# Kernel tuning notes

Measured on AMD Instinct MI355X. Metric: run time of the kernel, lower is better.

Reference implementation:

```python
import jax, jax.numpy as jnp
import numpy as np

B, T, D = 32, 1024, 192
HIDDEN = 4
CH = D * HIDDEN          # conv hidden channels = in_channel * hidden_size
K1, K2 = 5, 3
PAD = 3                  # (K1 - 1) // 2 + 1 for odd kernel_size=5 (ReplicationPad1d)
NUM_LEVELS = 3
N_NODES = 2 ** NUM_LEVELS - 1  # 7 Interaction blocks in the SCINet tree
OUT_LEN = 512


def setup_inputs() -> dict:
    key = jax.random.key(0)
    ks = jax.random.split(key, 6)
    s1 = 1.0 / np.sqrt(D * K1)   # torch Conv1d default init bound (fan_in = Cin*k)
    s2 = 1.0 / np.sqrt(CH * K2)
    sp = 1.0 / np.sqrt(T)
    x = jax.random.normal(ks[0], (B, T, D), dtype=jnp.float32)
    # Stacked params for all 7 tree nodes x 4 branches (phi, psi, eta, rho)
    W1 = jax.random.uniform(ks[1], (N_NODES, 4, CH, D, K1), jnp.float32, -s1, s1)
    b1 = jax.random.uniform(ks[2], (N_NODES, 4, CH), jnp.float32, -s1, s1)
    W2 = jax.random.uniform(ks[3], (N_NODES, 4, D, CH, K2), jnp.float32, -s2, s2)
    b2 = jax.random.uniform(ks[4], (N_NODES, 4, D), jnp.float32, -s2, s2)
    # projection1 = Conv1d(input_len, output_len, k=1, bias=False) over time-as-channels
    Wproj = jax.random.uniform(ks[5], (OUT_LEN, T), jnp.float32, -sp, sp)
    return {"x": x, "W1": W1, "b1": b1, "W2": W2, "b2": b2, "Wproj": Wproj}


def _conv1d(x, w, b):
    # x: (B, Cin, L), w: (Cout, Cin, K)
    y = jax.lax.conv_general_dilated(x, w, (1,), 'VALID',
                                     dimension_numbers=('NCH', 'OIH', 'NCH'))
    return y + b[None, :, None]


def _branch(x, w1, b1, w2, b2):
    # ReplicationPad1d(3,3) -> Conv(k=5) -> LeakyReLU -> (Dropout p=0) -> Conv(k=3) -> Tanh
    xp = jnp.pad(x, ((0, 0), (0, 0), (PAD, PAD)), mode='edge')
    h = jax.nn.leaky_relu(_conv1d(xp, w1, b1), 0.01)
    return jnp.tanh(_conv1d(h, w2, b2))  # length back to L


def _interact(x, w1, b1, w2, b2):
    # x: (B, T, D) -> even/odd (B, D, T/2)
    xe = jnp.transpose(x[:, ::2, :], (0, 2, 1))
    xo = jnp.transpose(x[:, 1::2, :], (0, 2, 1))
    d = xo * jnp.exp(_branch(xe, w1[0], b1[0], w2[0], b2[0]))  # phi
    c = xe * jnp.exp(_branch(xo, w1[1], b1[1], w2[1], b2[1]))  # psi
    even_up = c + _branch(d, w1[2], b1[2], w2[2], b2[2])        # eta
    odd_up = d - _branch(c, w1[3], b1[3], w2[3], b2[3])         # rho
    return jnp.transpose(even_up, (0, 2, 1)), jnp.transpose(odd_up, (0, 2, 1))


def _zip_up(even, odd):
    # interleave even/odd along time (equal lengths since T % 2**levels == 0)
    b, t, c = even.shape
    return jnp.stack([even, odd], axis=2).reshape(b, 2 * t, c)


def _tree(x, level, idx, W1, b1, W2, b2):
    i = idx[0]
    idx[0] += 1
    e, o = _interact(x, W1[i], b1[i], W2[i], b2[i])
    if level == 0:
        return _zip_up(e, o)
    return _zip_up(_tree(e, level - 1, idx, W1, b1, W2, b2),
                   _tree(o, level - 1, idx, W1, b1, W2, b2))


def reference(x, W1, b1, W2, b2, Wproj):
    out = _tree(x, NUM_LEVELS - 1, [0], W1, b1, W2, b2) + x  # residual
    # projection1: Conv1d over time-as-channels, kernel 1, no bias
    return jnp.einsum('btd,ot->bod', out, Wproj)
```

## Files before the change

### kernel.cpp

```cpp
#include <hip/hip_runtime.h>
#include <hip/hip_bf16.h>

typedef unsigned short u16;
typedef unsigned int u32;
typedef __bf16 bf16x8 __attribute__((ext_vector_type(8)));
typedef float f32x4 __attribute__((ext_vector_type(4)));

#define NB 32
#define NT 1024
#define ND 192
#define NCH 768
#define NOUT 512

__device__ __forceinline__ float bf2f(u16 x) { return __uint_as_float(((u32)x) << 16); }
__device__ __forceinline__ u16 f2bf(float f) {
    u32 u = __float_as_uint(f);
    return (u16)((u + 0x7fffu + ((u >> 16) & 1u)) >> 16);
}
__device__ __forceinline__ float tanh_fast(float x) {
    float e = __expf(2.f * x);
    return 1.f - 2.f / (e + 1.f);
}
__device__ __forceinline__ int xcd_swz(int bx, int nwg) {
    int q = nwg >> 3, r = nwg & 7;
    int xcd = bx & 7, idx = bx >> 3;
    return (xcd < r ? xcd * (q + 1) : r * (q + 1) + (xcd - r) * q) + idx;
}

__constant__ int NODE_IDX[3][4] = {{0, 0, 0, 0}, {1, 4, 0, 0}, {2, 5, 3, 6}};

__global__ void cvt8(const float* __restrict__ in, u16* __restrict__ out, int n8) {
    int i = blockIdx.x * 256 + threadIdx.x;
    if (i >= n8) return;
    const float4* p = (const float4*)in + 2 * (size_t)i;
    float4 a = p[0], c = p[1];
    uint4 o;
    o.x = f2bf(a.x) | ((u32)f2bf(a.y) << 16);
    o.y = f2bf(a.z) | ((u32)f2bf(a.w) << 16);
    o.z = f2bf(c.x) | ((u32)f2bf(c.y) << 16);
    o.w = f2bf(c.z) | ((u32)f2bf(c.w) << 16);
    ((uint4*)out)[i] = o;
}

__global__ __launch_bounds__(256) void w1fk(const float* __restrict__ W1, u16* __restrict__ W1f) {
    __shared__ u16 ls[32][968];
    const int nb = blockIdx.x / 24;
    const int cot = blockIdx.x % 24;
    const float* src = W1 + ((size_t)nb * NCH + cot * 32) * (ND * 5);
    for (int idx = threadIdx.x; idx < 7680; idx += 256) {
        int e4 = idx * 4;
        int rowc = e4 / 960, col = e4 % 960;
        float4 v = *(const float4*)(src + (size_t)rowc * 960 + col);
        ls[rowc][col + 0] = f2bf(v.x);
        ls[rowc][col + 1] = f2bf(v.y);
        ls[rowc][col + 2] = f2bf(v.z);
        ls[rowc][col + 3] = f2bf(v.w);
    }
    __syncthreads();
    const int lane = threadIdx.x & 63, sub = threadIdx.x >> 6;
    const int g = lane >> 4, r = lane & 15;
    for (int it = 0; it < 15; ++it) {
        int fid = it * 4 + sub;
        int kkb = fid >> 1, cobl = fid & 1;
        u16 tmp[8];
#pragma unroll
        for (int e = 0; e < 8; ++e) {
            int kk = kkb * 32 + 8 * g + e;
            int ci = kk % 192, k = kk / 192;
            tmp[e] = ls[cobl * 16 + r][ci * 5 + k];
        }
        uint4 o;
        o.x = tmp[0] | ((u32)tmp[1] << 16);
        o.y = tmp[2] | ((u32)tmp[3] << 16);
        o.z = tmp[4] | ((u32)tmp[5] << 16);
        o.w = tmp[6] | ((u32)tmp[7] << 16);
        size_t off = (((size_t)nb * 30 + kkb) * 48 + cot * 2 + cobl) * 512 + lane * 8;
        *(uint4*)(W1f + off) = o;
    }
}

__global__ __launch_bounds__(256) void w2fk(const float* __restrict__ W2, u16* __restrict__ W2f) {
    __shared__ u16 ls[16][1160];
    const int ch = blockIdx.x & 1;
    const int t = blockIdx.x >> 1;
    const int nb = t / 12, cot = t % 12;
    const float* src = W2 + ((size_t)nb * ND + cot * 16) * (NCH * 3) + ch * 1152;
    for (int idx = threadIdx.x; idx < 4608; idx += 256) {
        int e4 = idx * 4;
        int rowc = e4 / 1152, col = e4 % 1152;
        float4 v = *(const float4*)(src + (size_t)rowc * (NCH * 3) + col);
        ls[rowc][col + 0] = f2bf(v.x);
        ls[rowc][col + 1] = f2bf(v.y);
        ls[rowc][col + 2] = f2bf(v.z);
        ls[rowc][col + 3] = f2bf(v.w);
    }
    __syncthreads();
    const int lane = threadIdx.x & 63, sub = threadIdx.x >> 6;
    const int g = lane >> 4, r = lane & 15;
    for (int it = 0; it < 9; ++it) {
        int fid = it * 4 + sub;
        int k = fid / 12, cib = fid % 12;
        int kkb = k * 24 + ch * 12 + cib;
        u16 tmp[8];
#pragma unroll
        for (int e = 0; e < 8; ++e) {
            int cl = cib * 32 + 8 * g + e;
            tmp[e] = ls[r][cl * 3 + k];
        }
        uint4 o;
        o.x = tmp[0] | ((u32)tmp[1] << 16);
        o.y = tmp[2] | ((u32)tmp[3] << 16);
        o.z = tmp[4] | ((u32)tmp[5] << 16);
        o.w = tmp[6] | ((u32)tmp[7] << 16);
        size_t off = (((size_t)nb * 72 + kkb) * 12 + cot) * 512 + lane * 8;
        *(uint4*)(W2f + off) = o;
    }
}

__global__ __launch_bounds__(256) void conv1m(
    const u16* __restrict__ bufb, const u16* __restrict__ dbufb, const u16* __restrict__ cbufb,
    const u16* __restrict__ W1f, const float* __restrict__ b1,
    u16* __restrict__ h, int lvl, int stage) {
    const int L = 512 >> lvl, nodes = 1 << lvl, Lout = L + 2;
    const int tid = threadIdx.x;
    const int mT1 = (NB * Lout + 63) / 64;
    const int wg = xcd_swz(blockIdx.x, gridDim.x);
    const int z = wg / (6 * mT1);
    const int rem = wg - z * 6 * mT1;
    const int mt = rem / 6;
    const int cot = rem % 6;
    const int g_node = z & (nodes - 1);
    const int br = z >> lvl;
    const int nb4 = NODE_IDX[lvl][g_node] * 4 + (stage ? 2 + br : br);

    const int r0 = mt * 64;
    const int b0 = r0 / Lout;
    const int t00 = r0 - b0 * Lout;
    const int s = Lout - t00;
    const int rowsValid0 = NB * Lout - r0;
    const int rowsValid = rowsValid0 < 64 ? rowsValid0 : 64;

    __shared__ u16 xs[72 * 192];

    const u16* dcb = br ? cbufb : dbufb;
    const int slot = g_node + (br << lvl);
    for (int ch = tid; ch < 72 * 24; ch += 256) {
        int j = ch / 24, c8 = ch % 24;
        int bb, u;
        if (j <= s + 3) { bb = b0; u = t00 - 3 + j; }
        else            { bb = b0 + 1; u = j - s - 7; }
        u = u < 0 ? 0 : (u > L - 1 ? L - 1 : u);
        if (bb > NB - 1) bb = NB - 1;
        const u16* p;
        if (stage == 0)
            p = bufb + ((size_t)bb * NT + slot + (size_t)u * (2 * nodes)) * ND + c8 * 8;
        else
            p = dcb + (((size_t)g_node * NB + bb) * L + u) * (size_t)ND + c8 * 8;
        *(uint4*)(xs + j * 192 + ((c8 * 8) ^ ((j & 7) << 3))) = *(const uint4*)p;
    }
    __syncthreads();

    const int lane = tid & 63, w = tid >> 6;
    const int lr = lane & 15, lg = lane >> 4;

    int rowb[4];
#pragma unroll
    for (int m = 0; m < 4; ++m) {
        int i = m * 16 + lr;
        rowb[m] = i + (i >= s ? 4 : 0);
    }
    const u16* wf = W1f + (size_t)nb4 * 30 * 48 * 512 + (size_t)(cot * 8 + w * 2) * 512 + lane * 8;

    f32x4 acc[4][2];
    f32x4 zz = {0.f, 0.f, 0.f, 0.f};
#pragma unroll
    for (int m = 0; m < 4; ++m)
#pragma unroll
        for (int n = 0; n < 2; ++n) acc[m][n] = zz;

    auto loadA = [&](bf16x8(&dst)[4], int step) {
        const int k = step / 6, cib = step % 6;
#pragma unroll
        for (int m = 0; m < 4; ++m) {
            int row = rowb[m] + k;
            int idx = row * 192 + ((cib * 32 + lg * 8) ^ ((row & 7) << 3));
            dst[m] = *(const bf16x8*)(xs + idx);
        }
    };
    auto loadB = [&](bf16x8(&dst)[2], int step) {
#pragma unroll
        for (int n = 0; n < 2; ++n)
            dst[n] = *(const bf16x8*)(wf + ((size_t)step * 48 + n) * 512);
    };
    auto domfma = [&](bf16x8(&A)[4], bf16x8(&B)[2]) {
#pragma unroll
        for (int m = 0; m < 4; ++m)
#pragma unroll
            for (int n = 0; n < 2; ++n)
                acc[m][n] = __builtin_amdgcn_mfma_f32_16x16x32_bf16(A[m], B[n], acc[m][n], 0, 0, 0);
    };

    bf16x8 Ab[2][4], Bb[3][2];
    loadA(Ab[0], 0);
    loadB(Bb[0], 0);
    loadB(Bb[1], 1);
#pragma unroll
    for (int sp = 0; sp < 30; ++sp) {
        if (sp + 2 < 30) loadB(Bb[(sp + 2) % 3], sp + 2);
        if (sp + 1 < 30) loadA(Ab[(sp + 1) & 1], sp + 1);
        domfma(Ab[sp & 1], Bb[sp % 3]);
    }

    float bias[2];
    const float* bb1 = b1 + (size_t)nb4 * NCH + cot * 128 + w * 32 + lr;
#pragma unroll
    for (int n = 0; n < 2; ++n) bias[n] = bb1[n * 16];
    u16* hz = h + (size_t)z * NB * Lout * NCH;
#pragma unroll
    for (int m = 0; m < 4; ++m) {
#pragma unroll
        for (int rr = 0; rr < 4; ++rr) {
            int i = m * 16 + lg * 4 + rr;
            if (i < rowsValid) {
                int cross = (i >= s) ? 1 : 0;
                int bb = b0 + cross;
                int tt = cross ? i - s : t00 + i;
                u16* dst = hz + ((size_t)bb * Lout + tt) * NCH + cot * 128 + w * 32 + lr;
#pragma unroll
                for (int n = 0; n < 2; ++n) {
                    float v = acc[m][n][rr] + bias[n];
                    v = v > 0.f ? v : 0.01f * v;
                    dst[n * 16] = f2bf(v);
                }
            }
        }
    }
}

__global__ __launch_bounds__(256) void conv2m(
    u16* __restrict__ bufb, u16* __restrict__ dbufb, u16* __restrict__ cbufb,
    const u16* __restrict__ W2f, const float* __restrict__ b2,
    const u16* __restrict__ h, int lvl, int stage) {
    const int L = 512 >> lvl, nodes = 1 << lvl, Lout = L + 2;
    const int tid = threadIdx.x;
    const int nM = (NB * L) >> 6;
    const int wg = xcd_swz(blockIdx.x, gridDim.x);
    const int z = wg / (nM * 2);
    const int rem = wg - z * nM * 2;
    const int mt = rem >> 1;
    const int nh = rem & 1;
    const int g_node = z & (nodes - 1);
    const int br = z >> lvl;
    const int nb4 = NODE_IDX[lvl][g_node] * 4 + (stage ? 2 + br : br);
    const int r0 = mt * 64;
    const int b = r0 >> (9 - lvl);
    const int t0 = r0 & (L - 1);

    __shared__ u16 xs[66 * 192];
    const u16* hz = h + ((size_t)z * NB + b) * Lout * NCH;

    const int lane = tid & 63, w = tid >> 6;
    const int wrow = w >> 1, wcol = w & 1;
    const int lr = lane & 15, lg = lane >> 4;
    int rowb[2];
#pragma unroll
    for (int m = 0; m < 2; ++m) rowb[m] = wrow * 32 + m * 16 + lr;
    const u16* wf = W2f + (size_t)nb4 * 72 * 12 * 512 + (size_t)(nh * 6 + wcol * 3) * 512 + lane * 8;

    f32x4 acc[2][3];
    f32x4 zz = {0.f, 0.f, 0.f, 0.f};
#pragma unroll
    for (int m = 0; m < 2; ++m)
#pragma unroll
        for (int n = 0; n < 3; ++n) acc[m][n] = zz;

    for (int cc = 0; cc < 4; ++cc) {
        __syncthreads();
        for (int ch = tid; ch < 66 * 24; ch += 256) {
            int j = ch / 24, c8 = ch % 24;
            *(uint4*)(xs + j * 192 + ((c8 * 8) ^ ((j & 7) << 3))) =
                *(const uint4*)(hz + (size_t)(t0 + j) * NCH + cc * 192 + c8 * 8);
        }
        __syncthreads();

        auto loadA = [&](bf16x8(&dst)[2], int step) {
            const int k = step / 6, cib = step % 6;
#pragma unroll
            for (int m = 0; m < 2; ++m) {
                int row = rowb[m] + k;
                int idx = row * 192 + ((cib * 32 + lg * 8) ^ ((row & 7) << 3));
                dst[m] = *(const bf16x8*)(xs + idx);
            }
        };
        auto loadB = [&](bf16x8(&dst)[3], int step) {
            const int k = step / 6, cib = step % 6;
            const size_t kb = (size_t)(cc * 6 + k * 24 + cib) * 12 * 512;
#pragma unroll
            for (int n = 0; n < 3; ++n)
                dst[n] = *(const bf16x8*)(wf + kb + (size_t)n * 512);
        };
        auto domfma = [&](bf16x8(&A)[2], bf16x8(&B)[3]) {
#pragma unroll
            for (int m = 0; m < 2; ++m)
#pragma unroll
                for (int n = 0; n < 3; ++n)
                    acc[m][n] = __builtin_amdgcn_mfma_f32_16x16x32_bf16(A[m], B[n], acc[m][n], 0, 0, 0);
        };

        bf16x8 Ab[2][2], Bb[3][3];
        loadA(Ab[0], 0);
        loadB(Bb[0], 0);
        loadB(Bb[1], 1);
#pragma unroll
        for (int sp = 0; sp < 18; ++sp) {
            if (sp + 2 < 18) loadB(Bb[(sp + 2) % 3], sp + 2);
            if (sp + 1 < 18) loadA(Ab[(sp + 1) & 1], sp + 1);
            domfma(Ab[sp & 1], Bb[sp % 3]);
        }
    }

    float bias[3];
    const float* bb2 = b2 + (size_t)nb4 * ND + nh * 96 + wcol * 48 + lr;
#pragma unroll
    for (int n = 0; n < 3; ++n) bias[n] = bb2[n * 16];

    const int tstr = 2 * nodes;
    if (stage == 0) {
        const int mo = g_node + (br == 0 ? nodes : 0);
        const u16* mult = bufb + ((size_t)b * NT + mo) * ND;
        u16* dst = (br == 0 ? dbufb : cbufb) + ((size_t)g_node * NB + b) * (size_t)L * ND;
#pragma unroll
        for (int m = 0; m < 2; ++m) {
#pragma unroll
            for (int rr = 0; rr < 4; ++rr) {
                int i = wrow * 32 + m * 16 + lg * 4 + rr;
                int t = t0 + i;
#pragma unroll
                for (int n = 0; n < 3; ++n) {
                    int co = nh * 96 + wcol * 48 + n * 16 + lr;
                    float v = tanh_fast(acc[m][n][rr] + bias[n]);
                    float mlt = bf2f(mult[(size_t)t * tstr * ND + co]);
                    dst[(size_t)t * ND + co] = f2bf(mlt * __expf(v));
                }
            }
        }
    } else {
        const u16* other = (br == 0 ? cbufb : dbufb) + ((size_t)g_node * NB + b) * (size_t)L * ND;
        const int to = g_node + (br ? nodes : 0);
        u16* dst = bufb + ((size_t)b * NT + to) * ND;
#pragma unroll
        for (int m = 0; m < 2; ++m) {
#pragma unroll
            for (int rr = 0; rr < 4; ++rr) {
                int i = wrow * 32 + m * 16 + lg * 4 + rr;
                int t = t0 + i;
#pragma unroll
                for (int n = 0; n < 3; ++n) {
                    int co = nh * 96 + wcol * 48 + n * 16 + lr;
                    float v = tanh_fast(acc[m][n][rr] + bias[n]);
                    float o = bf2f(other[(size_t)t * ND + co]);
                    dst[(size_t)t * tstr * ND + co] = f2bf(br == 0 ? o + v : o - v);
                }
            }
        }
    }
}

__global__ __launch_bounds__(256) void mkin2T(const u16* __restrict__ bufb,
                                              const float* __restrict__ x,
                                              u16* __restrict__ in2T) {
    __shared__ u16 ls[64][72];
    const int b = blockIdx.z, t0 = blockIdx.y * 64, d0 = blockIdx.x * 64;
    const int tid = threadIdx.x;
#pragma unroll
    for (int it = 0; it < 2; ++it) {
        int idx = tid + it * 256;
        int c8 = idx >> 6, row = idx & 63;
        size_t base = ((size_t)b * NT + t0 + row) * ND + d0 + c8 * 8;
        uint4 vb = *(const uint4*)(bufb + base);
        float4 x1 = *(const float4*)(x + base);
        float4 x2 = *(const float4*)(x + base + 4);
        const u16* vs = (const u16*)&vb;
        ls[c8 * 8 + 0][row] = f2bf(bf2f(vs[0]) + x1.x);
        ls[c8 * 8 + 1][row] = f2bf(bf2f(vs[1]) + x1.y);
        ls[c8 * 8 + 2][row] = f2bf(bf2f(vs[2]) + x1.z);
        ls[c8 * 8 + 3][row] = f2bf(bf2f(vs[3]) + x1.w);
        ls[c8 * 8 + 4][row] = f2bf(bf2f(vs[4]) + x2.x);
        ls[c8 * 8 + 5][row] = f2bf(bf2f(vs[5]) + x2.y);
        ls[c8 * 8 + 6][row] = f2bf(bf2f(vs[6]) + x2.z);
        ls[c8 * 8 + 7][row] = f2bf(bf2f(vs[7]) + x2.w);
    }
    __syncthreads();
#pragma unroll
    for (int it = 0; it < 2; ++it) {
        int idx = tid + it * 256;
        int dl = idx >> 3, t8 = idx & 7;
        uint4 v = *(uint4*)&ls[dl][t8 * 8];
        *(uint4*)(in2T + ((size_t)b * ND + d0 + dl) * NT + t0 + t8 * 8) = v;
    }
}

__global__ __launch_bounds__(256) void projm(const u16* __restrict__ in2T,
                                             const u16* __restrict__ Wpb,
                                             float* __restrict__ out) {
    const int b = blockIdx.y, ot = blockIdx.x;
    const int tid = threadIdx.x, lane = tid & 63, w = tid >> 6;
    const int lr = lane & 15, lg = lane >> 4;
    const u16* ap = Wpb + ((size_t)(ot * 32 + lr)) * NT + lg * 8;
    const u16* bp = in2T + ((size_t)b * ND + w * 48 + lr) * NT + lg * 8;

    f32x4 acc[2][3];
    f32x4 zz = {0.f, 0.f, 0.f, 0.f};
#pragma unroll
    for (int m = 0; m < 2; ++m)
#pragma unroll
        for (int n = 0; n < 3; ++n) acc[m][n] = zz;

    auto loadA = [&](bf16x8(&dst)[2], int kkb) {
#pragma unroll
        for (int m = 0; m < 2; ++m)
            dst[m] = *(const bf16x8*)(ap + (size_t)m * 16 * NT + kkb * 32);
    };
    auto loadB = [&](bf16x8(&dst)[3], int kkb) {
#pragma unroll
        for (int n = 0; n < 3; ++n)
            dst[n] = *(const bf16x8*)(bp + (size_t)n * 16 * NT + kkb * 32);
    };
    auto domfma = [&](bf16x8(&A)[2], bf16x8(&B)[3]) {
#pragma unroll
        for (int m = 0; m < 2; ++m)
#pragma unroll
            for (int n = 0; n < 3; ++n)
                acc[m][n] = __builtin_amdgcn_mfma_f32_16x16x32_bf16(A[m], B[n], acc[m][n], 0, 0, 0);
    };

    bf16x8 Ab[2][2], Bb[3][3];
    loadA(Ab[0], 0);
    loadB(Bb[0], 0);
    loadB(Bb[1], 1);
#pragma unroll
    for (int sp = 0; sp < 32; ++sp) {
        if (sp + 2 < 32) loadB(Bb[(sp + 2) % 3], sp + 2);
        if (sp + 1 < 32) loadA(Ab[(sp + 1) & 1], sp + 1);
        domfma(Ab[sp & 1], Bb[sp % 3]);
    }

#pragma unroll
    for (int m = 0; m < 2; ++m)
#pragma unroll
        for (int rr = 0; rr < 4; ++rr) {
            int o = ot * 32 + m * 16 + lg * 4 + rr;
#pragma unroll
            for (int n = 0; n < 3; ++n) {
                int d = w * 48 + n * 16 + lr;
                out[((size_t)b * NOUT + o) * ND + d] = acc[m][n][rr];
            }
        }
}

extern "C" void kernel_launch(void* const* d_in, const int* in_sizes, int n_in,
                              void* d_out, int out_size, void* d_ws, size_t ws_size,
                              hipStream_t stream) {
    const float* x = (const float*)d_in[0];
    const float* W1 = (const float*)d_in[1];
    const float* b1 = (const float*)d_in[2];
    const float* W2 = (const float*)d_in[3];
    const float* b2 = (const float*)d_in[4];
    const float* Wp = (const float*)d_in[5];
    float* out = (float*)d_out;

    char* wsb = (char*)d_ws;
    size_t off = 0;
    auto carve = [&](size_t bytes) {
        void* p = wsb + off;
        off += (bytes + 255) & ~(size_t)255;
        return p;
    };
    const size_t w1f_e = (size_t)28 * 30 * 48 * 512;
    const size_t w2f_e = (size_t)28 * 72 * 12 * 512;
    const size_t wpb_e = (size_t)NOUT * NT;
    const size_t buf_e = (size_t)NB * NT * ND;
    const size_t dc_e = (size_t)NB * 512 * ND;
    const size_t h_e = (size_t)1040 * NB * NCH;
    const size_t i2_e = (size_t)NB * ND * NT;

    u16* W1f = (u16*)carve(sizeof(u16) * w1f_e);
    u16* W2f = (u16*)carve(sizeof(u16) * w2f_e);
    u16* Wpb = (u16*)carve(sizeof(u16) * wpb_e);
    u16* bufb = (u16*)carve(sizeof(u16) * buf_e);
    u16* dbufb = (u16*)carve(sizeof(u16) * dc_e);
    u16* cbufb = (u16*)carve(sizeof(u16) * dc_e);
    u16* h = (u16*)carve(sizeof(u16) * h_e);
    u16* in2T = (u16*)carve(sizeof(u16) * i2_e);
    if (off > ws_size) return;

    cvt8<<<(int)(buf_e / 8 / 256), 256, 0, stream>>>(x, bufb, (int)(buf_e / 8));
    cvt8<<<(int)(wpb_e / 8 / 256), 256, 0, stream>>>(Wp, Wpb, (int)(wpb_e / 8));
    w1fk<<<28 * 24, 256, 0, stream>>>(W1, W1f);
    w2fk<<<28 * 12 * 2, 256, 0, stream>>>(W2, W2f);

    for (int lvl = 0; lvl < 3; ++lvl) {
        int L = 512 >> lvl, nodes = 1 << lvl, Lout = L + 2;
        int mT1 = (NB * Lout + 63) / 64;
        int nM = NB * L / 64;
        dim3 g1(6 * mT1 * 2 * nodes);
        dim3 g2(nM * 2 * 2 * nodes);
        conv1m<<<g1, 256, 0, stream>>>(bufb, dbufb, cbufb, W1f, b1, h, lvl, 0);
        conv2m<<<g2, 256, 0, stream>>>(bufb, dbufb, cbufb, W2f, b2, h, lvl, 0);
        conv1m<<<g1, 256, 0, stream>>>(bufb, dbufb, cbufb, W1f, b1, h, lvl, 1);
        conv2m<<<g2, 256, 0, stream>>>(bufb, dbufb, cbufb, W2f, b2, h, lvl, 1);
    }
    mkin2T<<<dim3(3, 16, NB), 256, 0, stream>>>(bufb, x, in2T);
    projm<<<dim3(16, NB), 256, 0, stream>>>(in2T, Wpb, out);
}
```

Measured before the change: 778.4 us.

## Enlarge conv GEMM tiles and stage weights into LDS via direct global-to-LDS loads

conv1m now computes 128-row by 128-channel tiles, with four waves in a 2x2 grid, where it used 64 rows. conv2m drops the output-channel split so each block covers all 192 output channels over 64 rows. In both kernels the weight fragments are double-buffered in LDS using global_load_lds, so one staged B tile is shared by all waves instead of each wave reading it from global memory. The aim is fewer weight reloads per FLOP and fewer A-tile rebuilds, at the cost of a __syncthreads on every k-step, more LDS, fewer blocks and added launch-bounds occupancy hints.

```diff
diff --git a/kernel.cpp b/kernel.cpp
--- a/kernel.cpp
+++ b/kernel.cpp
@@ -25,6 +25,11 @@
     int q = nwg >> 3, r = nwg & 7;
     int xcd = bx & 7, idx = bx >> 3;
     return (xcd < r ? xcd * (q + 1) : r * (q + 1) + (xcd - r) * q) + idx;
+}
+__device__ __forceinline__ void gl_lds16(const u16* g, u16* l) {
+    __builtin_amdgcn_global_load_lds(
+        (const __attribute__((address_space(1))) void*)g,
+        (__attribute__((address_space(3))) void*)l, 16, 0, 0);
 }
 
 __constant__ int NODE_IDX[3][4] = {{0, 0, 0, 0}, {1, 4, 0, 0}, {2, 5, 3, 6}};
@@ -117,13 +122,13 @@
     }
 }
 
-__global__ __launch_bounds__(256) void conv1m(
+__global__ __launch_bounds__(256, 2) void conv1m(
     const u16* __restrict__ bufb, const u16* __restrict__ dbufb, const u16* __restrict__ cbufb,
     const u16* __restrict__ W1f, const float* __restrict__ b1,
     u16* __restrict__ h, int lvl, int stage) {
     const int L = 512 >> lvl, nodes = 1 << lvl, Lout = L + 2;
     const int tid = threadIdx.x;
-    const int mT1 = (NB * Lout + 63) / 64;
+    const int mT1 = (NB * Lout + 127) / 128;
     const int wg = xcd_swz(blockIdx.x, gridDim.x);
     const int z = wg / (6 * mT1);
     const int rem = wg - z * 6 * mT1;
@@ -133,18 +138,19 @@
     const int br = z >> lvl;
     const int nb4 = NODE_IDX[lvl][g_node] * 4 + (stage ? 2 + br : br);
 
-    const int r0 = mt * 64;
+    const int r0 = mt * 128;
     const int b0 = r0 / Lout;
     const int t00 = r0 - b0 * Lout;
     const int s = Lout - t00;
     const int rowsValid0 = NB * Lout - r0;
-    const int rowsValid = rowsValid0 < 64 ? rowsValid0 : 64;
-
-    __shared__ u16 xs[72 * 192];
+    const int rowsValid = rowsValid0 < 128 ? rowsValid0 : 128;
+
+    __shared__ u16 xs[136 * 192];
+    __shared__ u16 bs[2][4096];
 
     const u16* dcb = br ? cbufb : dbufb;
     const int slot = g_node + (br << lvl);
-    for (int ch = tid; ch < 72 * 24; ch += 256) {
+    for (int ch = tid; ch < 136 * 24; ch += 256) {
         int j = ch / 24, c8 = ch % 24;
         int bb, u;
         if (j <= s + 3) { bb = b0; u = t00 - 3 + j; }
@@ -158,76 +164,73 @@
             p = dcb + (((size_t)g_node * NB + bb) * L + u) * (size_t)ND + c8 * 8;
         *(uint4*)(xs + j * 192 + ((c8 * 8) ^ ((j & 7) << 3))) = *(const uint4*)p;
     }
+
+    const u16* wsrc = W1f + ((size_t)nb4 * 30 * 48 + cot * 8) * 512;
+    auto stageB = [&](int kkb, int buf) {
+        const u16* gp = wsrc + (size_t)kkb * (48 * 512) + tid * 8;
+        u16* lp = &bs[buf][tid * 8];
+        gl_lds16(gp, lp);
+        gl_lds16(gp + 2048, lp + 2048);
+    };
+    stageB(0, 0);
     __syncthreads();
 
     const int lane = tid & 63, w = tid >> 6;
+    const int wrow = w >> 1, wcol = w & 1;
     const int lr = lane & 15, lg = lane >> 4;
 
     int rowb[4];
 #pragma unroll
     for (int m = 0; m < 4; ++m) {
-        int i = m * 16 + lr;
+        int i = wrow * 64 + m * 16 + lr;
         rowb[m] = i + (i >= s ? 4 : 0);
     }
-    const u16* wf = W1f + (size_t)nb4 * 30 * 48 * 512 + (size_t)(cot * 8 + w * 2) * 512 + lane * 8;
-
-    f32x4 acc[4][2];
+
+    f32x4 acc[4][4];
     f32x4 zz = {0.f, 0.f, 0.f, 0.f};
 #pragma unroll
     for (int m = 0; m < 4; ++m)
 #pragma unroll
-        for (int n = 0; n < 2; ++n) acc[m][n] = zz;
-
-    auto loadA = [&](bf16x8(&dst)[4], int step) {
-        const int k = step / 6, cib = step % 6;
+        for (int n = 0; n < 4; ++n) acc[m][n] = zz;
+
+#pragma unroll
+    for (int kkb = 0; kkb < 30; ++kkb) {
+        if (kkb < 29) stageB(kkb + 1, (kkb + 1) & 1);
+        const int k = kkb / 6, cib = kkb % 6;
+        bf16x8 Af[4], Bf[4];
 #pragma unroll
         for (int m = 0; m < 4; ++m) {
             int row = rowb[m] + k;
-            int idx = row * 192 + ((cib * 32 + lg * 8) ^ ((row & 7) << 3));
-            dst[m] = *(const bf16x8*)(xs + idx);
-        }
-    };
-    auto loadB = [&](bf16x8(&dst)[2], int step) {
-#pragma unroll
-        for (int n = 0; n < 2; ++n)
-            dst[n] = *(const bf16x8*)(wf + ((size_t)step * 48 + n) * 512);
-    };
-    auto domfma = [&](bf16x8(&A)[4], bf16x8(&B)[2]) {
+            Af[m] = *(const bf16x8*)(xs + row * 192 + ((cib * 32 + lg * 8) ^ ((row & 7) << 3)));
+        }
+#pragma unroll
+        for (int n = 0; n < 4; ++n)
+            Bf[n] = *(const bf16x8*)(&bs[kkb & 1][(wcol * 4 + n) * 512 + lane * 8]);
 #pragma unroll
         for (int m = 0; m < 4; ++m)
 #pragma unroll
-            for (int n = 0; n < 2; ++n)
-                acc[m][n] = __builtin_amdgcn_mfma_f32_16x16x32_bf16(A[m], B[n], acc[m][n], 0, 0, 0);
-    };
-
-    bf16x8 Ab[2][4], Bb[3][2];
-    loadA(Ab[0], 0);
-    loadB(Bb[0], 0);
-    loadB(Bb[1], 1);
-#pragma unroll
-    for (int sp = 0; sp < 30; ++sp) {
-        if (sp + 2 < 30) loadB(Bb[(sp + 2) % 3], sp + 2);
-        if (sp + 1 < 30) loadA(Ab[(sp + 1) & 1], sp + 1);
-        domfma(Ab[sp & 1], Bb[sp % 3]);
-    }
-
-    float bias[2];
-    const float* bb1 = b1 + (size_t)nb4 * NCH + cot * 128 + w * 32 + lr;
-#pragma unroll
-    for (int n = 0; n < 2; ++n) bias[n] = bb1[n * 16];
+            for (int n = 0; n < 4; ++n)
+                acc[m][n] = __builtin_amdgcn_mfma_f32_16x16x32_bf16(Af[m], Bf[n], acc[m][n], 0, 0, 0);
+        __syncthreads();
+    }
+
+    float bias[4];
+    const float* bb1 = b1 + (size_t)nb4 * NCH + cot * 128 + wcol * 64 + lr;
+#pragma unroll
+    for (int n = 0; n < 4; ++n) bias[n] = bb1[n * 16];
     u16* hz = h + (size_t)z * NB * Lout * NCH;
 #pragma unroll
     for (int m = 0; m < 4; ++m) {
 #pragma unroll
         for (int rr = 0; rr < 4; ++rr) {
-            int i = m * 16 + lg * 4 + rr;
+            int i = wrow * 64 + m * 16 + lg * 4 + rr;
             if (i < rowsValid) {
                 int cross = (i >= s) ? 1 : 0;
                 int bb = b0 + cross;
                 int tt = cross ? i - s : t00 + i;
-                u16* dst = hz + ((size_t)bb * Lout + tt) * NCH + cot * 128 + w * 32 + lr;
-#pragma unroll
-                for (int n = 0; n < 2; ++n) {
+                u16* dst = hz + ((size_t)bb * Lout + tt) * NCH + cot * 128 + wcol * 64 + lr;
+#pragma unroll
+                for (int n = 0; n < 4; ++n) {
                     float v = acc[m][n][rr] + bias[n];
                     v = v > 0.f ? v : 0.01f * v;
                     dst[n * 16] = f2bf(v);
@@ -237,7 +240,7 @@
     }
 }
 
-__global__ __launch_bounds__(256) void conv2m(
+__global__ __launch_bounds__(256, 3) void conv2m(
     u16* __restrict__ bufb, u16* __restrict__ dbufb, u16* __restrict__ cbufb,
     const u16* __restrict__ W2f, const float* __restrict__ b2,
     const u16* __restrict__ h, int lvl, int stage) {
@@ -245,10 +248,8 @@
     const int tid = threadIdx.x;
     const int nM = (NB * L) >> 6;
     const int wg = xcd_swz(blockIdx.x, gridDim.x);
-    const int z = wg / (nM * 2);
-    const int rem = wg - z * nM * 2;
-    const int mt = rem >> 1;
-    const int nh = rem & 1;
+    const int z = wg / nM;
+    const int mt = wg - z * nM;
     const int g_node = z & (nodes - 1);
     const int br = z >> lvl;
     const int nb4 = NODE_IDX[lvl][g_node] * 4 + (stage ? 2 + br : br);
@@ -257,70 +258,64 @@
     const int t0 = r0 & (L - 1);
 
     __shared__ u16 xs[66 * 192];
+    __shared__ u16 bs[2][6144];
     const u16* hz = h + ((size_t)z * NB + b) * Lout * NCH;
 
     const int lane = tid & 63, w = tid >> 6;
-    const int wrow = w >> 1, wcol = w & 1;
     const int lr = lane & 15, lg = lane >> 4;
-    int rowb[2];
-#pragma unroll
-    for (int m = 0; m < 2; ++m) rowb[m] = wrow * 32 + m * 16 + lr;
-    const u16* wf = W2f + (size_t)nb4 * 72 * 12 * 512 + (size_t)(nh * 6 + wcol * 3) * 512 + lane * 8;
-
-    f32x4 acc[2][3];
+
+    const u16* wsrc = W2f + (size_t)nb4 * 72 * 12 * 512;
+    auto stageB = [&](int kkb, int buf) {
+        const u16* gp = wsrc + (size_t)kkb * (12 * 512) + tid * 8;
+        u16* lp = &bs[buf][tid * 8];
+        gl_lds16(gp, lp);
+        gl_lds16(gp + 2048, lp + 2048);
+        gl_lds16(gp + 4096, lp + 4096);
+    };
+
+    f32x4 acc[4][3];
     f32x4 zz = {0.f, 0.f, 0.f, 0.f};
 #pragma unroll
-    for (int m = 0; m < 2; ++m)
+    for (int m = 0; m < 4; ++m)
 #pragma unroll
         for (int n = 0; n < 3; ++n) acc[m][n] = zz;
 
     for (int cc = 0; cc < 4; ++cc) {
         __syncthreads();
+        stageB(cc * 6, 0);
         for (int ch = tid; ch < 66 * 24; ch += 256) {
             int j = ch / 24, c8 = ch % 24;
             *(uint4*)(xs + j * 192 + ((c8 * 8) ^ ((j & 7) << 3))) =
                 *(const uint4*)(hz + (size_t)(t0 + j) * NCH + cc * 192 + c8 * 8);
         }
         __syncthreads();
-
-        auto loadA = [&](bf16x8(&dst)[2], int step) {
-            const int k = step / 6, cib = step % 6;
-#pragma unroll
-            for (int m = 0; m < 2; ++m) {
-                int row = rowb[m] + k;
-                int idx = row * 192 + ((cib * 32 + lg * 8) ^ ((row & 7) << 3));
-                dst[m] = *(const bf16x8*)(xs + idx);
+#pragma unroll
+        for (int sp = 0; sp < 18; ++sp) {
+            if (sp < 17) {
+                int spn = sp + 1;
+                stageB((spn / 6) * 24 + cc * 6 + (spn % 6), spn & 1);
             }
-        };
-        auto loadB = [&](bf16x8(&dst)[3], int step) {
-            const int k = step / 6, cib = step % 6;
-            const size_t kb = (size_t)(cc * 6 + k * 24 + cib) * 12 * 512;
+            const int k = sp / 6, cib = sp % 6;
+            bf16x8 Af[4], Bf[3];
+#pragma unroll
+            for (int m = 0; m < 4; ++m) {
+                int row = m * 16 + lr + k;
+                Af[m] = *(const bf16x8*)(xs + row * 192 + ((cib * 32 + lg * 8) ^ ((row & 7) << 3)));
+            }
 #pragma unroll
             for (int n = 0; n < 3; ++n)
-                dst[n] = *(const bf16x8*)(wf + kb + (size_t)n * 512);
-        };
-        auto domfma = [&](bf16x8(&A)[2], bf16x8(&B)[3]) {
-#pragma unroll
-            for (int m = 0; m < 2; ++m)
+                Bf[n] = *(const bf16x8*)(&bs[sp & 1][(w * 3 + n) * 512 + lane * 8]);
+#pragma unroll
+            for (int m = 0; m < 4; ++m)
 #pragma unroll
                 for (int n = 0; n < 3; ++n)
-                    acc[m][n] = __builtin_amdgcn_mfma_f32_16x16x32_bf16(A[m], B[n], acc[m][n], 0, 0, 0);
-        };
-
-        bf16x8 Ab[2][2], Bb[3][3];
-        loadA(Ab[0], 0);
-        loadB(Bb[0], 0);
-        loadB(Bb[1], 1);
-#pragma unroll
-        for (int sp = 0; sp < 18; ++sp) {
-            if (sp + 2 < 18) loadB(Bb[(sp + 2) % 3], sp + 2);
-            if (sp + 1 < 18) loadA(Ab[(sp + 1) & 1], sp + 1);
-            domfma(Ab[sp & 1], Bb[sp % 3]);
+                    acc[m][n] = __builtin_amdgcn_mfma_f32_16x16x32_bf16(Af[m], Bf[n], acc[m][n], 0, 0, 0);
+            __syncthreads();
         }
     }
 
     float bias[3];
-    const float* bb2 = b2 + (size_t)nb4 * ND + nh * 96 + wcol * 48 + lr;
+    const float* bb2 = b2 + (size_t)nb4 * ND + w * 48 + lr;
 #pragma unroll
     for (int n = 0; n < 3; ++n) bias[n] = bb2[n * 16];
 
@@ -330,14 +325,14 @@
         const u16* mult = bufb + ((size_t)b * NT + mo) * ND;
         u16* dst = (br == 0 ? dbufb : cbufb) + ((size_t)g_node * NB + b) * (size_t)L * ND;
 #pragma unroll
-        for (int m = 0; m < 2; ++m) {
+        for (int m = 0; m < 4; ++m) {
 #pragma unroll
             for (int rr = 0; rr < 4; ++rr) {
-                int i = wrow * 32 + m * 16 + lg * 4 + rr;
+                int i = m * 16 + lg * 4 + rr;
                 int t = t0 + i;
 #pragma unroll
                 for (int n = 0; n < 3; ++n) {
-                    int co = nh * 96 + wcol * 48 + n * 16 + lr;
+                    int co = w * 48 + n * 16 + lr;
                     float v = tanh_fast(acc[m][n][rr] + bias[n]);
                     float mlt = bf2f(mult[(size_t)t * tstr * ND + co]);
                     dst[(size_t)t * ND + co] = f2bf(mlt * __expf(v));
@@ -349,14 +344,14 @@
         const int to = g_node + (br ? nodes : 0);
         u16* dst = bufb + ((size_t)b * NT + to) * ND;
 #pragma unroll
-        for (int m = 0; m < 2; ++m) {
+        for (int m = 0; m < 4; ++m) {
 #pragma unroll
             for (int rr = 0; rr < 4; ++rr) {
-                int i = wrow * 32 + m * 16 + lg * 4 + rr;
+                int i = m * 16 + lg * 4 + rr;
                 int t = t0 + i;
 #pragma unroll
                 for (int n = 0; n < 3; ++n) {
-                    int co = nh * 96 + wcol * 48 + n * 16 + lr;
+                    int co = w * 48 + n * 16 + lr;
                     float v = tanh_fast(acc[m][n][rr] + bias[n]);
                     float o = bf2f(other[(size_t)t * ND + co]);
                     dst[(size_t)t * tstr * ND + co] = f2bf(br == 0 ? o + v : o - v);
@@ -501,10 +496,10 @@
 
     for (int lvl = 0; lvl < 3; ++lvl) {
         int L = 512 >> lvl, nodes = 1 << lvl, Lout = L + 2;
-        int mT1 = (NB * Lout + 63) / 64;
+        int mT1 = (NB * Lout + 127) / 128;
         int nM = NB * L / 64;
         dim3 g1(6 * mT1 * 2 * nodes);
-        dim3 g2(nM * 2 * 2 * nodes);
+        dim3 g2(nM * 2 * nodes);
         conv1m<<<g1, 256, 0, stream>>>(bufb, dbufb, cbufb, W1f, b1, h, lvl, 0);
         conv2m<<<g2, 256, 0, stream>>>(bufb, dbufb, cbufb, W2f, b2, h, lvl, 0);
         conv1m<<<g1, 256, 0, stream>>>(bufb, dbufb, cbufb, W1f, b1, h, lvl, 1);
```

After: 927.7 us. 19.2% more time.

## Switch conv GEMMs to 32x32x16 MFMA with larger tiles and repacked weights

Applied to the files above, without the earlier changes.

Both convolution GEMM kernels move from 16x16x32 to 32x32x16 bf16 MFMA instructions, and the weight-prepacking kernels are rewritten to emit fragments in the matching 32-row layout. conv1m doubles its M tile to 128 rows, which raises reuse of the shared input tile. conv2m drops the N-half split, so each block computes all 192 output channels and the hidden activations are loaded once instead of twice. The larger tiles give fewer workgroups and higher register and LDS use per block, which may reduce occupancy at the smaller tree levels.

```diff
diff --git a/kernel.cpp b/kernel.cpp
--- a/kernel.cpp
+++ b/kernel.cpp
@@ -5,6 +5,7 @@
 typedef unsigned int u32;
 typedef __bf16 bf16x8 __attribute__((ext_vector_type(8)));
 typedef float f32x4 __attribute__((ext_vector_type(4)));
+typedef float f32x16 __attribute__((ext_vector_type(16)));
 
 #define NB 32
 #define NT 1024
@@ -58,36 +59,35 @@
     }
     __syncthreads();
     const int lane = threadIdx.x & 63, sub = threadIdx.x >> 6;
-    const int g = lane >> 4, r = lane & 15;
+    const int r = lane & 31, g = lane >> 5;
     for (int it = 0; it < 15; ++it) {
-        int fid = it * 4 + sub;
-        int kkb = fid >> 1, cobl = fid & 1;
+        int kkb2 = it * 4 + sub;
         u16 tmp[8];
 #pragma unroll
         for (int e = 0; e < 8; ++e) {
-            int kk = kkb * 32 + 8 * g + e;
+            int kk = kkb2 * 16 + 8 * g + e;
             int ci = kk % 192, k = kk / 192;
-            tmp[e] = ls[cobl * 16 + r][ci * 5 + k];
+            tmp[e] = ls[r][ci * 5 + k];
         }
         uint4 o;
         o.x = tmp[0] | ((u32)tmp[1] << 16);
         o.y = tmp[2] | ((u32)tmp[3] << 16);
         o.z = tmp[4] | ((u32)tmp[5] << 16);
         o.w = tmp[6] | ((u32)tmp[7] << 16);
-        size_t off = (((size_t)nb * 30 + kkb) * 48 + cot * 2 + cobl) * 512 + lane * 8;
+        size_t off = (((size_t)nb * 60 + kkb2) * 24 + cot) * 512 + lane * 8;
         *(uint4*)(W1f + off) = o;
     }
 }
 
 __global__ __launch_bounds__(256) void w2fk(const float* __restrict__ W2, u16* __restrict__ W2f) {
-    __shared__ u16 ls[16][1160];
-    const int ch = blockIdx.x & 1;
-    const int t = blockIdx.x >> 1;
-    const int nb = t / 12, cot = t % 12;
-    const float* src = W2 + ((size_t)nb * ND + cot * 16) * (NCH * 3) + ch * 1152;
+    __shared__ u16 ls[32][579];
+    const int nb = blockIdx.x / 24;
+    const int rem = blockIdx.x % 24;
+    const int cob2 = rem / 4, ch = rem % 4;
+    const float* src = W2 + ((size_t)nb * ND + cob2 * 32) * (NCH * 3) + ch * 576;
     for (int idx = threadIdx.x; idx < 4608; idx += 256) {
         int e4 = idx * 4;
-        int rowc = e4 / 1152, col = e4 % 1152;
+        int rowc = e4 / 576, col = e4 % 576;
         float4 v = *(const float4*)(src + (size_t)rowc * (NCH * 3) + col);
         ls[rowc][col + 0] = f2bf(v.x);
         ls[rowc][col + 1] = f2bf(v.y);
@@ -96,23 +96,23 @@
     }
     __syncthreads();
     const int lane = threadIdx.x & 63, sub = threadIdx.x >> 6;
-    const int g = lane >> 4, r = lane & 15;
+    const int r = lane & 31, g = lane >> 5;
     for (int it = 0; it < 9; ++it) {
         int fid = it * 4 + sub;
-        int k = fid / 12, cib = fid % 12;
-        int kkb = k * 24 + ch * 12 + cib;
+        int k = fid / 12, cj = fid % 12;
+        int kkb2 = k * 48 + ch * 12 + cj;
         u16 tmp[8];
 #pragma unroll
         for (int e = 0; e < 8; ++e) {
-            int cl = cib * 32 + 8 * g + e;
-            tmp[e] = ls[r][cl * 3 + k];
+            int c_loc = cj * 16 + 8 * g + e;
+            tmp[e] = ls[r][c_loc * 3 + k];
         }
         uint4 o;
         o.x = tmp[0] | ((u32)tmp[1] << 16);
         o.y = tmp[2] | ((u32)tmp[3] << 16);
         o.z = tmp[4] | ((u32)tmp[5] << 16);
         o.w = tmp[6] | ((u32)tmp[7] << 16);
-        size_t off = (((size_t)nb * 72 + kkb) * 12 + cot) * 512 + lane * 8;
+        size_t off = (((size_t)nb * 144 + kkb2) * 6 + cob2) * 512 + lane * 8;
         *(uint4*)(W2f + off) = o;
     }
 }
@@ -123,7 +123,7 @@
     u16* __restrict__ h, int lvl, int stage) {
     const int L = 512 >> lvl, nodes = 1 << lvl, Lout = L + 2;
     const int tid = threadIdx.x;
-    const int mT1 = (NB * Lout + 63) / 64;
+    const int mT1 = (NB * Lout + 127) / 128;
     const int wg = xcd_swz(blockIdx.x, gridDim.x);
     const int z = wg / (6 * mT1);
     const int rem = wg - z * 6 * mT1;
@@ -133,18 +133,18 @@
     const int br = z >> lvl;
     const int nb4 = NODE_IDX[lvl][g_node] * 4 + (stage ? 2 + br : br);
 
-    const int r0 = mt * 64;
+    const int r0 = mt * 128;
     const int b0 = r0 / Lout;
     const int t00 = r0 - b0 * Lout;
     const int s = Lout - t00;
     const int rowsValid0 = NB * Lout - r0;
-    const int rowsValid = rowsValid0 < 64 ? rowsValid0 : 64;
-
-    __shared__ u16 xs[72 * 192];
+    const int rowsValid = rowsValid0 < 128 ? rowsValid0 : 128;
+
+    __shared__ u16 xs[136 * 192];
 
     const u16* dcb = br ? cbufb : dbufb;
     const int slot = g_node + (br << lvl);
-    for (int ch = tid; ch < 72 * 24; ch += 256) {
+    for (int ch = tid; ch < 136 * 24; ch += 256) {
         int j = ch / 24, c8 = ch % 24;
         int bb, u;
         if (j <= s + 3) { bb = b0; u = t00 - 3 + j; }
@@ -158,79 +158,80 @@
             p = dcb + (((size_t)g_node * NB + bb) * L + u) * (size_t)ND + c8 * 8;
         *(uint4*)(xs + j * 192 + ((c8 * 8) ^ ((j & 7) << 3))) = *(const uint4*)p;
     }
+
+    const int lane = tid & 63, w = tid >> 6;
+    const int wrow = w >> 1, wcol = w & 1;
+    const int l31 = lane & 31, lg2 = lane >> 5;
+
+    int rowb[2];
+#pragma unroll
+    for (int m = 0; m < 2; ++m) {
+        int i = wrow * 64 + m * 32 + l31;
+        rowb[m] = i + (i >= s ? 4 : 0);
+    }
+    const u16* wf = W1f + ((size_t)nb4 * 60 * 24 + cot * 4 + wcol * 2) * 512 + lane * 8;
+
     __syncthreads();
 
-    const int lane = tid & 63, w = tid >> 6;
-    const int lr = lane & 15, lg = lane >> 4;
-
-    int rowb[4];
-#pragma unroll
-    for (int m = 0; m < 4; ++m) {
-        int i = m * 16 + lr;
-        rowb[m] = i + (i >= s ? 4 : 0);
-    }
-    const u16* wf = W1f + (size_t)nb4 * 30 * 48 * 512 + (size_t)(cot * 8 + w * 2) * 512 + lane * 8;
-
-    f32x4 acc[4][2];
-    f32x4 zz = {0.f, 0.f, 0.f, 0.f};
-#pragma unroll
-    for (int m = 0; m < 4; ++m)
-#pragma unroll
-        for (int n = 0; n < 2; ++n) acc[m][n] = zz;
-
-    auto loadA = [&](bf16x8(&dst)[4], int step) {
-        const int k = step / 6, cib = step % 6;
-#pragma unroll
-        for (int m = 0; m < 4; ++m) {
-            int row = rowb[m] + k;
-            int idx = row * 192 + ((cib * 32 + lg * 8) ^ ((row & 7) << 3));
-            dst[m] = *(const bf16x8*)(xs + idx);
-        }
-    };
-    auto loadB = [&](bf16x8(&dst)[2], int step) {
+    f32x16 acc[2][2];
+#pragma unroll
+    for (int m = 0; m < 2; ++m)
+#pragma unroll
+        for (int n = 0; n < 2; ++n) acc[m][n] = (f32x16)0.f;
+
+    auto loadA = [&](bf16x8(&dst)[2], int st) {
+        const int kc = st / 12, cij = st % 12;
+        const int ci0 = cij * 16 + lg2 * 8;
+#pragma unroll
+        for (int m = 0; m < 2; ++m) {
+            int row = rowb[m] + kc;
+            dst[m] = *(const bf16x8*)(xs + row * 192 + (ci0 ^ ((row & 7) << 3)));
+        }
+    };
+    auto loadB = [&](bf16x8(&dst)[2], int st) {
 #pragma unroll
         for (int n = 0; n < 2; ++n)
-            dst[n] = *(const bf16x8*)(wf + ((size_t)step * 48 + n) * 512);
-    };
-    auto domfma = [&](bf16x8(&A)[4], bf16x8(&B)[2]) {
-#pragma unroll
-        for (int m = 0; m < 4; ++m)
-#pragma unroll
-            for (int n = 0; n < 2; ++n)
-                acc[m][n] = __builtin_amdgcn_mfma_f32_16x16x32_bf16(A[m], B[n], acc[m][n], 0, 0, 0);
-    };
-
-    bf16x8 Ab[2][4], Bb[3][2];
+            dst[n] = *(const bf16x8*)(wf + ((size_t)st * 24 + n) * 512);
+    };
+
+    bf16x8 Ab[2][2], Bb[4][2];
     loadA(Ab[0], 0);
     loadB(Bb[0], 0);
     loadB(Bb[1], 1);
-#pragma unroll
-    for (int sp = 0; sp < 30; ++sp) {
-        if (sp + 2 < 30) loadB(Bb[(sp + 2) % 3], sp + 2);
-        if (sp + 1 < 30) loadA(Ab[(sp + 1) & 1], sp + 1);
-        domfma(Ab[sp & 1], Bb[sp % 3]);
+    loadB(Bb[2], 2);
+#pragma unroll
+    for (int st = 0; st < 60; ++st) {
+        if (st + 3 < 60) loadB(Bb[(st + 3) & 3], st + 3);
+        if (st + 1 < 60) loadA(Ab[(st + 1) & 1], st + 1);
+#pragma unroll
+        for (int m = 0; m < 2; ++m)
+#pragma unroll
+            for (int n = 0; n < 2; ++n)
+                acc[m][n] = __builtin_amdgcn_mfma_f32_32x32x16_bf16(
+                    Ab[st & 1][m], Bb[st & 3][n], acc[m][n], 0, 0, 0);
     }
 
     float bias[2];
-    const float* bb1 = b1 + (size_t)nb4 * NCH + cot * 128 + w * 32 + lr;
-#pragma unroll
-    for (int n = 0; n < 2; ++n) bias[n] = bb1[n * 16];
+    const float* bb1 = b1 + (size_t)nb4 * NCH + cot * 128 + wcol * 64 + l31;
+#pragma unroll
+    for (int n = 0; n < 2; ++n) bias[n] = bb1[n * 32];
     u16* hz = h + (size_t)z * NB * Lout * NCH;
 #pragma unroll
-    for (int m = 0; m < 4; ++m) {
-#pragma unroll
-        for (int rr = 0; rr < 4; ++rr) {
-            int i = m * 16 + lg * 4 + rr;
+    for (int m = 0; m < 2; ++m) {
+#pragma unroll
+        for (int r = 0; r < 16; ++r) {
+            int row_local = (r & 3) + 8 * (r >> 2) + 4 * lg2;
+            int i = wrow * 64 + m * 32 + row_local;
             if (i < rowsValid) {
                 int cross = (i >= s) ? 1 : 0;
                 int bb = b0 + cross;
                 int tt = cross ? i - s : t00 + i;
-                u16* dst = hz + ((size_t)bb * Lout + tt) * NCH + cot * 128 + w * 32 + lr;
+                u16* dst = hz + ((size_t)bb * Lout + tt) * NCH + cot * 128 + wcol * 64 + l31;
 #pragma unroll
                 for (int n = 0; n < 2; ++n) {
-                    float v = acc[m][n][rr] + bias[n];
+                    float v = acc[m][n][r] + bias[n];
                     v = v > 0.f ? v : 0.01f * v;
-                    dst[n * 16] = f2bf(v);
+                    dst[n * 32] = f2bf(v);
                 }
             }
         }
@@ -245,10 +246,8 @@
     const int tid = threadIdx.x;
     const int nM = (NB * L) >> 6;
     const int wg = xcd_swz(blockIdx.x, gridDim.x);
-    const int z = wg / (nM * 2);
-    const int rem = wg - z * nM * 2;
-    const int mt = rem >> 1;
-    const int nh = rem & 1;
+    const int z = wg / nM;
+    const int mt = wg - z * nM;
     const int g_node = z & (nodes - 1);
     const int br = z >> lvl;
     const int nb4 = NODE_IDX[lvl][g_node] * 4 + (stage ? 2 + br : br);
@@ -261,18 +260,35 @@
 
     const int lane = tid & 63, w = tid >> 6;
     const int wrow = w >> 1, wcol = w & 1;
-    const int lr = lane & 15, lg = lane >> 4;
-    int rowb[2];
-#pragma unroll
-    for (int m = 0; m < 2; ++m) rowb[m] = wrow * 32 + m * 16 + lr;
-    const u16* wf = W2f + (size_t)nb4 * 72 * 12 * 512 + (size_t)(nh * 6 + wcol * 3) * 512 + lane * 8;
-
-    f32x4 acc[2][3];
-    f32x4 zz = {0.f, 0.f, 0.f, 0.f};
-#pragma unroll
-    for (int m = 0; m < 2; ++m)
-#pragma unroll
-        for (int n = 0; n < 3; ++n) acc[m][n] = zz;
+    const int l31 = lane & 31, lg2 = lane >> 5;
+
+    const u16* wf = W2f + ((size_t)nb4 * 144 * 6 + wcol * 3) * 512 + lane * 8;
+
+    f32x16 acc[3];
+#pragma unroll
+    for (int n = 0; n < 3; ++n) acc[n] = (f32x16)0.f;
+
+    auto kkb2_of = [](int st) {
+        int cc = st / 36, wi = st % 36, k = wi / 12, cj = wi % 12;
+        return k * 48 + cc * 12 + cj;
+    };
+    auto loadB = [&](bf16x8(&dst)[3], int st) {
+        const size_t kb = (size_t)kkb2_of(st) * 6 * 512;
+#pragma unroll
+        for (int n = 0; n < 3; ++n)
+            dst[n] = *(const bf16x8*)(wf + kb + (size_t)n * 512);
+    };
+    auto loadA = [&](bf16x8& dst, int wi) {
+        const int k = wi / 12, cj = wi % 12;
+        const int row = wrow * 32 + l31 + k;
+        const int ci0 = cj * 16 + lg2 * 8;
+        dst = *(const bf16x8*)(xs + row * 192 + (ci0 ^ ((row & 7) << 3)));
+    };
+
+    bf16x8 Bb[4][3], Af[2];
+    loadB(Bb[0], 0);
+    loadB(Bb[1], 1);
+    loadB(Bb[2], 2);
 
     for (int cc = 0; cc < 4; ++cc) {
         __syncthreads();
@@ -282,47 +298,23 @@
                 *(const uint4*)(hz + (size_t)(t0 + j) * NCH + cc * 192 + c8 * 8);
         }
         __syncthreads();
-
-        auto loadA = [&](bf16x8(&dst)[2], int step) {
-            const int k = step / 6, cib = step % 6;
-#pragma unroll
-            for (int m = 0; m < 2; ++m) {
-                int row = rowb[m] + k;
-                int idx = row * 192 + ((cib * 32 + lg * 8) ^ ((row & 7) << 3));
-                dst[m] = *(const bf16x8*)(xs + idx);
-            }
-        };
-        auto loadB = [&](bf16x8(&dst)[3], int step) {
-            const int k = step / 6, cib = step % 6;
-            const size_t kb = (size_t)(cc * 6 + k * 24 + cib) * 12 * 512;
+        loadA(Af[0], 0);
+#pragma unroll
+        for (int wi = 0; wi < 36; ++wi) {
+            int st = cc * 36 + wi;
+            if (st + 3 < 144) loadB(Bb[(st + 3) & 3], st + 3);
+            if (wi + 1 < 36) loadA(Af[(wi + 1) & 1], wi + 1);
 #pragma unroll
             for (int n = 0; n < 3; ++n)
-                dst[n] = *(const bf16x8*)(wf + kb + (size_t)n * 512);
-        };
-        auto domfma = [&](bf16x8(&A)[2], bf16x8(&B)[3]) {
-#pragma unroll
-            for (int m = 0; m < 2; ++m)
-#pragma unroll
-                for (int n = 0; n < 3; ++n)
-                    acc[m][n] = __builtin_amdgcn_mfma_f32_16x16x32_bf16(A[m], B[n], acc[m][n], 0, 0, 0);
-        };
-
-        bf16x8 Ab[2][2], Bb[3][3];
-        loadA(Ab[0], 0);
-        loadB(Bb[0], 0);
-        loadB(Bb[1], 1);
-#pragma unroll
-        for (int sp = 0; sp < 18; ++sp) {
-            if (sp + 2 < 18) loadB(Bb[(sp + 2) % 3], sp + 2);
-            if (sp + 1 < 18) loadA(Ab[(sp + 1) & 1], sp + 1);
-            domfma(Ab[sp & 1], Bb[sp % 3]);
+                acc[n] = __builtin_amdgcn_mfma_f32_32x32x16_bf16(
+                    Af[wi & 1], Bb[st & 3][n], acc[n], 0, 0, 0);
         }
     }
 
     float bias[3];
-    const float* bb2 = b2 + (size_t)nb4 * ND + nh * 96 + wcol * 48 + lr;
-#pragma unroll
-    for (int n = 0; n < 3; ++n) bias[n] = bb2[n * 16];
+    const float* bb2 = b2 + (size_t)nb4 * ND + wcol * 96 + l31;
+#pragma unroll
+    for (int n = 0; n < 3; ++n) bias[n] = bb2[n * 32];
 
     const int tstr = 2 * nodes;
     if (stage == 0) {
@@ -330,18 +322,15 @@
         const u16* mult = bufb + ((size_t)b * NT + mo) * ND;
         u16* dst = (br == 0 ? dbufb : cbufb) + ((size_t)g_node * NB + b) * (size_t)L * ND;
 #pragma unroll
-        for (int m = 0; m < 2; ++m) {
-#pragma unroll
-            for (int rr = 0; rr < 4; ++rr) {
-                int i = wrow * 32 + m * 16 + lg * 4 + rr;
-                int t = t0 + i;
-#pragma unroll
-                for (int n = 0; n < 3; ++n) {
-                    int co = nh * 96 + wcol * 48 + n * 16 + lr;
-                    float v = tanh_fast(acc[m][n][rr] + bias[n]);
-                    float mlt = bf2f(mult[(size_t)t * tstr * ND + co]);
-                    dst[(size_t)t * ND + co] = f2bf(mlt * __expf(v));
-                }
+        for (int r = 0; r < 16; ++r) {
+            int row_local = (r & 3) + 8 * (r >> 2) + 4 * lg2;
+            int t = t0 + wrow * 32 + row_local;
+#pragma unroll
+            for (int n = 0; n < 3; ++n) {
+                int co = wcol * 96 + n * 32 + l31;
+                float v = tanh_fast(acc[n][r] + bias[n]);
+                float mlt = bf2f(mult[(size_t)t * tstr * ND + co]);
+                dst[(size_t)t * ND + co] = f2bf(mlt * __expf(v));
             }
         }
     } else {
@@ -349,18 +338,15 @@
         const int to = g_node + (br ? nodes : 0);
         u16* dst = bufb + ((size_t)b * NT + to) * ND;
 #pragma unroll
-        for (int m = 0; m < 2; ++m) {
-#pragma unroll
-            for (int rr = 0; rr < 4; ++rr) {
-                int i = wrow * 32 + m * 16 + lg * 4 + rr;
-                int t = t0 + i;
-#pragma unroll
-                for (int n = 0; n < 3; ++n) {
-                    int co = nh * 96 + wcol * 48 + n * 16 + lr;
-                    float v = tanh_fast(acc[m][n][rr] + bias[n]);
-                    float o = bf2f(other[(size_t)t * ND + co]);
-                    dst[(size_t)t * tstr * ND + co] = f2bf(br == 0 ? o + v : o - v);
-                }
+        for (int r = 0; r < 16; ++r) {
+            int row_local = (r & 3) + 8 * (r >> 2) + 4 * lg2;
+            int t = t0 + wrow * 32 + row_local;
+#pragma unroll
+            for (int n = 0; n < 3; ++n) {
+                int co = wcol * 96 + n * 32 + l31;
+                float v = tanh_fast(acc[n][r] + bias[n]);
+                float o = bf2f(other[(size_t)t * ND + co]);
+                dst[(size_t)t * tstr * ND + co] = f2bf(br == 0 ? o + v : o - v);
             }
         }
     }
@@ -476,8 +462,8 @@
         off += (bytes + 255) & ~(size_t)255;
         return p;
     };
-    const size_t w1f_e = (size_t)28 * 30 * 48 * 512;
-    const size_t w2f_e = (size_t)28 * 72 * 12 * 512;
+    const size_t w1f_e = (size_t)28 * 60 * 24 * 512;
+    const size_t w2f_e = (size_t)28 * 144 * 6 * 512;
     const size_t wpb_e = (size_t)NOUT * NT;
     const size_t buf_e = (size_t)NB * NT * ND;
     const size_t dc_e = (size_t)NB * 512 * ND;
@@ -497,14 +483,14 @@
     cvt8<<<(int)(buf_e / 8 / 256), 256, 0, stream>>>(x, bufb, (int)(buf_e / 8));
     cvt8<<<(int)(wpb_e / 8 / 256), 256, 0, stream>>>(Wp, Wpb, (int)(wpb_e / 8));
     w1fk<<<28 * 24, 256, 0, stream>>>(W1, W1f);
-    w2fk<<<28 * 12 * 2, 256, 0, stream>>>(W2, W2f);
+    w2fk<<<28 * 24, 256, 0, stream>>>(W2, W2f);
 
     for (int lvl = 0; lvl < 3; ++lvl) {
         int L = 512 >> lvl, nodes = 1 << lvl, Lout = L + 2;
-        int mT1 = (NB * Lout + 63) / 64;
+        int mT1 = (NB * Lout + 127) / 128;
         int nM = NB * L / 64;
         dim3 g1(6 * mT1 * 2 * nodes);
-        dim3 g2(nM * 2 * 2 * nodes);
+        dim3 g2(nM * 2 * nodes);
         conv1m<<<g1, 256, 0, stream>>>(bufb, dbufb, cbufb, W1f, b1, h, lvl, 0);
         conv2m<<<g2, 256, 0, stream>>>(bufb, dbufb, cbufb, W2f, b2, h, lvl, 0);
         conv1m<<<g1, 256, 0, stream>>>(bufb, dbufb, cbufb, W1f, b1, h, lvl, 1);
```

After: 870.7 us. 1.12x slower.
